# Kernel optimization log

Hardware: AMD Instinct MI355X
Metric: run time of the kernel (lower is better)

The kernel has to match this reference:

```python
import jax, jax.numpy as jnp
import numpy as np

N_NODES = 50000
N_EDGES = 800000
D_FEAT = 64
UNITS = 64


def setup_inputs() -> dict:
    key = jax.random.key(0)
    k1, k2, k3, k4, k5 = jax.random.split(key, 5)
    node_feat = jax.random.normal(k1, (N_NODES, D_FEAT), dtype=jnp.float32)
    edge_feat = jax.random.normal(k2, (N_EDGES, D_FEAT), dtype=jnp.float32)
    src_idx = jax.random.randint(k3, (N_EDGES,), 0, N_NODES)
    tgt_idx = jax.random.randint(k4, (N_EDGES,), 0, N_NODES)
    # Dense kernel for the edge update: concat(src, tgt, edge) -> units
    W = jax.random.normal(k5, (3 * D_FEAT, UNITS), dtype=jnp.float32) / np.sqrt(3 * D_FEAT)
    b = jnp.zeros((UNITS,), dtype=jnp.float32)
    return {"node_feat": node_feat, "edge_feat": edge_feat,
            "src_idx": src_idx, "tgt_idx": tgt_idx, "W": W, "b": b}


def reference(node_feat, edge_feat, src_idx, tgt_idx, W, b):
    # EdgeSetUpdate: gather endpoint states, concat with edge feature, Dense+relu.
    # [n_edges, 3*d_feat]
    msg_in = jnp.concatenate([node_feat[src_idx], node_feat[tgt_idx], edge_feat], axis=-1)
    messages = jax.nn.relu(msg_in @ W + b)  # [n_edges, units]
    # pool_edges_to_node(..., TARGET, 'sum'): segment-sum messages to target nodes.
    pooled = jax.ops.segment_sum(messages, tgt_idx, num_segments=node_feat.shape[0])
    return pooled
```

## Files before the change

kernel.cpp:

```cpp
#include <hip/hip_runtime.h>
#include <hip/hip_bf16.h>


using s16x8 = __attribute__((ext_vector_type(8))) short;
using f32x4 = __attribute__((ext_vector_type(4))) float;

static __device__ __forceinline__ ushort f2bf(float f) {
    union { __hip_bfloat16 h; ushort u; } cv;
    cv.h = __float2bfloat16(f);
    return cv.u;
}

__global__ void prep_wt(const float* __restrict__ W, ushort* __restrict__ WT) {
    int idx = blockIdx.x * blockDim.x + threadIdx.x;
    if (idx < 64 * 192) {
        int n = idx / 192;
        int k = idx % 192;
        WT[idx] = f2bf(W[k * 64 + n]);
    }
}

__global__ __launch_bounds__(256) void edge_gemm(
    const float* __restrict__ node, const float* __restrict__ edgef,
    const int* __restrict__ src, const int* __restrict__ tgt,
    const ushort* __restrict__ WT, const float* __restrict__ bias,
    float* __restrict__ out, int n_edges)
{
    __shared__ __align__(16) ushort A[4][16][200];

    const int wave = threadIdx.x >> 6;
    const int lane = threadIdx.x & 63;
    const int g = lane >> 4;
    const int r = lane & 15;

    s16x8 Bf[4][6];
#pragma unroll
    for (int nt = 0; nt < 4; ++nt) {
#pragma unroll
        for (int ks = 0; ks < 6; ++ks) {
            const int n = nt * 16 + r;
            const int k0 = ks * 32 + g * 8;
            Bf[nt][ks] = *reinterpret_cast<const s16x8*>(WT + n * 192 + k0);
        }
    }
    float bv[4];
#pragma unroll
    for (int nt = 0; nt < 4; ++nt) bv[nt] = bias[nt * 16 + r];

    const int tile0 = blockIdx.x * 64 + wave * 16;

#pragma unroll
    for (int seg = 0; seg < 3; ++seg) {
#pragma unroll
        for (int i = 0; i < 4; ++i) {
            const int el = i * 4 + g;
            const int e = tile0 + el;
            const int ee = (e < n_edges) ? e : 0;
            const float* p;
            if (seg == 0)      p = node + (size_t)src[ee] * 64;
            else if (seg == 1) p = node + (size_t)tgt[ee] * 64;
            else               p = edgef + (size_t)ee * 64;
            const f32x4 v = *reinterpret_cast<const f32x4*>(p + r * 4);
            ushort4 h;
            h.x = f2bf(v[0]); h.y = f2bf(v[1]); h.z = f2bf(v[2]); h.w = f2bf(v[3]);
            *reinterpret_cast<ushort4*>(&A[wave][el][seg * 64 + r * 4]) = h;
        }
    }
    __syncthreads();

    f32x4 acc[4] = {{0.f,0.f,0.f,0.f},{0.f,0.f,0.f,0.f},{0.f,0.f,0.f,0.f},{0.f,0.f,0.f,0.f}};
#pragma unroll
    for (int ks = 0; ks < 6; ++ks) {
        const s16x8 a = *reinterpret_cast<const s16x8*>(&A[wave][r][ks * 32 + g * 8]);
#pragma unroll
        for (int nt = 0; nt < 4; ++nt) {
            acc[nt] = __builtin_amdgcn_mfma_f32_16x16x32_bf16(a, Bf[nt][ks], acc[nt], 0, 0, 0);
        }
    }

#pragma unroll
    for (int nt = 0; nt < 4; ++nt) {
        const int n = nt * 16 + r;
#pragma unroll
        for (int j = 0; j < 4; ++j) {
            const int row = g * 4 + j;
            const int e = tile0 + row;
            if (e < n_edges) {
                float v = fmaxf(acc[nt][j] + bv[nt], 0.0f);
                const int t = tgt[e];
                unsafeAtomicAdd(out + (size_t)t * 64 + n, v);
            }
        }
    }
}

extern "C" void kernel_launch(void* const* d_in, const int* in_sizes, int n_in,
                              void* d_out, int out_size, void* d_ws, size_t ws_size,
                              hipStream_t stream) {
    const float* node  = (const float*)d_in[0];
    const float* edgef = (const float*)d_in[1];
    const int*   src   = (const int*)d_in[2];
    const int*   tgt   = (const int*)d_in[3];
    const float* W     = (const float*)d_in[4];
    const float* bias  = (const float*)d_in[5];
    float* out = (float*)d_out;
    const int n_edges = in_sizes[2];

    ushort* WT = (ushort*)d_ws;

    hipMemsetAsync(d_out, 0, (size_t)out_size * sizeof(float), stream);
    prep_wt<<<48, 256, 0, stream>>>(W, WT);

    const int tiles = (n_edges + 63) / 64;
    edge_gemm<<<tiles, 256, 0, stream>>>(node, edgef, src, tgt, WT, bias, out, n_edges);
}
```

Measured before the change: 521.7 us.

## Replace atomic scatter with counting-sort CSR and segmented pooling of bf16 messages

Builds a CSR grouping of edges by target node through a histogram, a single-block scan and an atomic permutation build. The GEMM then processes edges in sorted order and writes bf16 messages to a workspace buffer. A separate pooling kernel sums each node's contiguous messages with no float atomics. This removes the 51M float atomics but adds several extra launches, a serial single-block scan over 50k nodes, a 100MB message round trip, and bf16 rounding of the messages before they are summed. The build order from atomics is nondeterministic, and if the workspace is too small the code falls back to the old atomic path.

```diff
diff --git a/kernel.cpp b/kernel.cpp
--- a/kernel.cpp
+++ b/kernel.cpp
@@ -9,6 +9,11 @@
     union { __hip_bfloat16 h; ushort u; } cv;
     cv.h = __float2bfloat16(f);
     return cv.u;
+}
+static __device__ __forceinline__ float bf2f(ushort u) {
+    union { unsigned u; float f; } cv;
+    cv.u = ((unsigned)u) << 16;
+    return cv.f;
 }
 
 __global__ void prep_wt(const float* __restrict__ W, ushort* __restrict__ WT) {
@@ -20,35 +25,172 @@
     }
 }
 
-__global__ __launch_bounds__(256) void edge_gemm(
+__global__ void hist_tgt(const int* __restrict__ tgt, int* __restrict__ counts, int n_edges) {
+    int i = blockIdx.x * blockDim.x + threadIdx.x;
+    if (i < n_edges) atomicAdd(&counts[tgt[i]], 1);
+}
+
+__global__ __launch_bounds__(1024) void scan_counts(
+    const int* __restrict__ counts, int* __restrict__ offsets, int* __restrict__ woff,
+    int n_nodes, int n_edges)
+{
+    __shared__ int wsum[16];
+    __shared__ int base_s;
+    const int tid = threadIdx.x, lane = tid & 63, wid = tid >> 6;
+    if (tid == 0) base_s = 0;
+    __syncthreads();
+    for (int c0 = 0; c0 < n_nodes; c0 += 1024) {
+        const int idx = c0 + tid;
+        const int v = (idx < n_nodes) ? counts[idx] : 0;
+        int x = v;
+#pragma unroll
+        for (int o = 1; o < 64; o <<= 1) { int t = __shfl_up(x, o, 64); if (lane >= o) x += t; }
+        if (lane == 63) wsum[wid] = x;
+        __syncthreads();
+        if (tid < 16) {
+            int w = wsum[tid];
+#pragma unroll
+            for (int o = 1; o < 16; o <<= 1) { int t = __shfl_up(w, o, 16); if (tid >= o) w += t; }
+            wsum[tid] = w;
+        }
+        __syncthreads();
+        const int wbase = (wid == 0) ? 0 : wsum[wid - 1];
+        const int excl = base_s + wbase + x - v;
+        if (idx < n_nodes) { offsets[idx] = excl; woff[idx] = excl; }
+        const int total = wsum[15];
+        __syncthreads();
+        if (tid == 0) base_s += total;
+        __syncthreads();
+    }
+    if (threadIdx.x == 0) offsets[n_nodes] = n_edges;
+}
+
+__global__ void build_perm(const int* __restrict__ tgt, int* __restrict__ woff,
+                           int* __restrict__ perm, int n_edges) {
+    int i = blockIdx.x * blockDim.x + threadIdx.x;
+    if (i < n_edges) {
+        int p = atomicAdd(&woff[tgt[i]], 1);
+        perm[p] = i;
+    }
+}
+
+__global__ __launch_bounds__(256) void edge_gemm_sorted(
+    const float* __restrict__ node, const float* __restrict__ edgef,
+    const int* __restrict__ src, const int* __restrict__ tgt,
+    const int* __restrict__ perm,
+    const ushort* __restrict__ WT, const float* __restrict__ bias,
+    ushort* __restrict__ msg, int n_edges)
+{
+    __shared__ __align__(16) ushort A[4][16][200];
+
+    const int wave = threadIdx.x >> 6;
+    const int lane = threadIdx.x & 63;
+    const int g = lane >> 4;
+    const int r = lane & 15;
+
+    s16x8 Bf[4][6];
+#pragma unroll
+    for (int nt = 0; nt < 4; ++nt)
+#pragma unroll
+        for (int ks = 0; ks < 6; ++ks)
+            Bf[nt][ks] = *reinterpret_cast<const s16x8*>(WT + (nt * 16 + r) * 192 + ks * 32 + g * 8);
+
+    float bv[4];
+#pragma unroll
+    for (int nt = 0; nt < 4; ++nt) bv[nt] = bias[nt * 16 + r];
+
+    const int tile0 = blockIdx.x * 64 + wave * 16;
+
+    int eidx[4], sidx[4], tidx[4];
+#pragma unroll
+    for (int i = 0; i < 4; ++i) {
+        int pos = tile0 + i * 4 + g;
+        if (pos >= n_edges) pos = n_edges - 1;
+        eidx[i] = perm[pos];
+    }
+#pragma unroll
+    for (int i = 0; i < 4; ++i) { sidx[i] = src[eidx[i]]; tidx[i] = tgt[eidx[i]]; }
+
+#pragma unroll
+    for (int seg = 0; seg < 3; ++seg) {
+#pragma unroll
+        for (int i = 0; i < 4; ++i) {
+            const int el = i * 4 + g;
+            const float* p;
+            if (seg == 0)      p = node + (size_t)sidx[i] * 64;
+            else if (seg == 1) p = node + (size_t)tidx[i] * 64;
+            else               p = edgef + (size_t)eidx[i] * 64;
+            const f32x4 v = *reinterpret_cast<const f32x4*>(p + r * 4);
+            ushort4 h;
+            h.x = f2bf(v[0]); h.y = f2bf(v[1]); h.z = f2bf(v[2]); h.w = f2bf(v[3]);
+            *reinterpret_cast<ushort4*>(&A[wave][el][seg * 64 + r * 4]) = h;
+        }
+    }
+    __syncthreads();
+
+    f32x4 acc[4] = {{0.f,0.f,0.f,0.f},{0.f,0.f,0.f,0.f},{0.f,0.f,0.f,0.f},{0.f,0.f,0.f,0.f}};
+#pragma unroll
+    for (int ks = 0; ks < 6; ++ks) {
+        const s16x8 a = *reinterpret_cast<const s16x8*>(&A[wave][r][ks * 32 + g * 8]);
+#pragma unroll
+        for (int nt = 0; nt < 4; ++nt)
+            acc[nt] = __builtin_amdgcn_mfma_f32_16x16x32_bf16(a, Bf[nt][ks], acc[nt], 0, 0, 0);
+    }
+
+    __syncthreads();
+#pragma unroll
+    for (int nt = 0; nt < 4; ++nt) {
+#pragma unroll
+        for (int j = 0; j < 4; ++j) {
+            const int row = g * 4 + j;
+            const float v = fmaxf(acc[nt][j] + bv[nt], 0.0f);
+            A[wave][row][nt * 16 + r] = f2bf(v);
+        }
+    }
+    __syncthreads();
+    const int row = lane >> 2, q = lane & 3;
+    if (tile0 + row < n_edges) {
+        const s16x8 m0 = *reinterpret_cast<const s16x8*>(&A[wave][row][q * 16]);
+        const s16x8 m1 = *reinterpret_cast<const s16x8*>(&A[wave][row][q * 16 + 8]);
+        const size_t p = (size_t)(tile0 + row) * 64 + q * 16;
+        *reinterpret_cast<s16x8*>(msg + p) = m0;
+        *reinterpret_cast<s16x8*>(msg + p + 8) = m1;
+    }
+}
+
+__global__ __launch_bounds__(256) void pool_msgs(
+    const ushort* __restrict__ msg, const int* __restrict__ offsets,
+    float* __restrict__ out, int n_nodes)
+{
+    const int wave = threadIdx.x >> 6, lane = threadIdx.x & 63;
+    const int n = blockIdx.x * 4 + wave;
+    if (n >= n_nodes) return;
+    const int s = offsets[n], e = offsets[n + 1];
+    float acc = 0.f;
+    for (int i = s; i < e; ++i) acc += bf2f(msg[(size_t)i * 64 + lane]);
+    out[(size_t)n * 64 + lane] = acc;
+}
+
+__global__ __launch_bounds__(256) void edge_gemm_atomic(
     const float* __restrict__ node, const float* __restrict__ edgef,
     const int* __restrict__ src, const int* __restrict__ tgt,
     const ushort* __restrict__ WT, const float* __restrict__ bias,
     float* __restrict__ out, int n_edges)
 {
     __shared__ __align__(16) ushort A[4][16][200];
-
     const int wave = threadIdx.x >> 6;
     const int lane = threadIdx.x & 63;
-    const int g = lane >> 4;
-    const int r = lane & 15;
-
+    const int g = lane >> 4, r = lane & 15;
     s16x8 Bf[4][6];
 #pragma unroll
-    for (int nt = 0; nt < 4; ++nt) {
-#pragma unroll
-        for (int ks = 0; ks < 6; ++ks) {
-            const int n = nt * 16 + r;
-            const int k0 = ks * 32 + g * 8;
-            Bf[nt][ks] = *reinterpret_cast<const s16x8*>(WT + n * 192 + k0);
-        }
-    }
+    for (int nt = 0; nt < 4; ++nt)
+#pragma unroll
+        for (int ks = 0; ks < 6; ++ks)
+            Bf[nt][ks] = *reinterpret_cast<const s16x8*>(WT + (nt * 16 + r) * 192 + ks * 32 + g * 8);
     float bv[4];
 #pragma unroll
     for (int nt = 0; nt < 4; ++nt) bv[nt] = bias[nt * 16 + r];
-
     const int tile0 = blockIdx.x * 64 + wave * 16;
-
 #pragma unroll
     for (int seg = 0; seg < 3; ++seg) {
 #pragma unroll
@@ -67,17 +209,14 @@
         }
     }
     __syncthreads();
-
     f32x4 acc[4] = {{0.f,0.f,0.f,0.f},{0.f,0.f,0.f,0.f},{0.f,0.f,0.f,0.f},{0.f,0.f,0.f,0.f}};
 #pragma unroll
     for (int ks = 0; ks < 6; ++ks) {
         const s16x8 a = *reinterpret_cast<const s16x8*>(&A[wave][r][ks * 32 + g * 8]);
 #pragma unroll
-        for (int nt = 0; nt < 4; ++nt) {
+        for (int nt = 0; nt < 4; ++nt)
             acc[nt] = __builtin_amdgcn_mfma_f32_16x16x32_bf16(a, Bf[nt][ks], acc[nt], 0, 0, 0);
-        }
-    }
-
+    }
 #pragma unroll
     for (int nt = 0; nt < 4; ++nt) {
         const int n = nt * 16 + r;
@@ -87,8 +226,7 @@
             const int e = tile0 + row;
             if (e < n_edges) {
                 float v = fmaxf(acc[nt][j] + bv[nt], 0.0f);
-                const int t = tgt[e];
-                unsafeAtomicAdd(out + (size_t)t * 64 + n, v);
+                unsafeAtomicAdd(out + (size_t)tgt[e] * 64 + n, v);
             }
         }
     }
@@ -105,12 +243,39 @@
     const float* bias  = (const float*)d_in[5];
     float* out = (float*)d_out;
     const int n_edges = in_sizes[2];
-
-    ushort* WT = (ushort*)d_ws;
-
-    hipMemsetAsync(d_out, 0, (size_t)out_size * sizeof(float), stream);
+    const int n_nodes = in_sizes[0] / 64;
+
+    char* ws = (char*)d_ws;
+    size_t cur = 0;
+    auto take = [&](size_t b) { size_t s = cur; cur = (cur + b + 255) & ~(size_t)255; return s; };
+    const size_t oWT   = take((size_t)64 * 192 * 2);
+    const size_t oCnt  = take((size_t)n_nodes * 4);
+    const size_t oOff  = take((size_t)(n_nodes + 1) * 4);
+    const size_t oWoff = take((size_t)n_nodes * 4);
+    const size_t oPerm = take((size_t)n_edges * 4);
+    const size_t oMsg  = take((size_t)n_edges * 64 * 2);
+    const bool sorted_ok = (cur <= ws_size);
+
+    ushort* WT = (ushort*)(ws + oWT);
     prep_wt<<<48, 256, 0, stream>>>(W, WT);
 
-    const int tiles = (n_edges + 63) / 64;
-    edge_gemm<<<tiles, 256, 0, stream>>>(node, edgef, src, tgt, WT, bias, out, n_edges);
-}
+    if (sorted_ok) {
+        int* counts  = (int*)(ws + oCnt);
+        int* offsets = (int*)(ws + oOff);
+        int* woff    = (int*)(ws + oWoff);
+        int* perm    = (int*)(ws + oPerm);
+        ushort* msg  = (ushort*)(ws + oMsg);
+
+        hipMemsetAsync(counts, 0, (size_t)n_nodes * 4, stream);
+        hist_tgt<<<(n_edges + 255) / 256, 256, 0, stream>>>(tgt, counts, n_edges);
+        scan_counts<<<1, 1024, 0, stream>>>(counts, offsets, woff, n_nodes, n_edges);
+        build_perm<<<(n_edges + 255) / 256, 256, 0, stream>>>(tgt, woff, perm, n_edges);
+        edge_gemm_sorted<<<(n_edges + 63) / 64, 256, 0, stream>>>(
+            node, edgef, src, tgt, perm, WT, bias, msg, n_edges);
+        pool_msgs<<<(n_nodes + 3) / 4, 256, 0, stream>>>(msg, offsets, out, n_nodes);
+    } else {
+        hipMemsetAsync(d_out, 0, (size_t)out_size * sizeof(float), stream);
+        edge_gemm_atomic<<<(n_edges + 63) / 64, 256, 0, stream>>>(
+            node, edgef, src, tgt, WT, bias, out, n_edges);
+    }
+}
```

Measured after the change: 620.8 us. +19.0%, slower.
